# Performance work log

Measured on AMD Instinct MI355X. Metric: run time of the kernel, lower is better.

The kernel has to match this reference:

```python
import jax, jax.numpy as jnp
import numpy as np

N, E, G = 50000, 1600000, 512
IN_DIM, HEADS, C1, C2, HIDDEN = 128, 3, 32, 32, 512
NEG_SLOPE = 0.2
EPS = 1e-16


def _glorot(key, shape):
    fan_in = shape[0]
    return jax.random.normal(key, shape, dtype=jnp.float32) / np.sqrt(fan_in)


def setup_inputs() -> dict:
    key = jax.random.key(0)
    ks = jax.random.split(key, 16)
    x = jax.random.normal(ks[0], (N, IN_DIM), dtype=jnp.float32)
    edge_index = jax.random.randint(ks[1], (2, E), 0, N, dtype=jnp.int64)
    batch = (jnp.arange(N, dtype=jnp.int64) * G) // N  # sorted, all graphs non-empty
    d1, d2 = HEADS * C1, HEADS * C2
    return {
        "x": x,
        "W_l1": _glorot(ks[2], (IN_DIM, d1)), "b_l1": jnp.zeros((d1,), jnp.float32),
        "W_r1": _glorot(ks[3], (IN_DIM, d1)), "b_r1": jnp.zeros((d1,), jnp.float32),
        "att1": _glorot(ks[4], (HEADS, C1)), "bias1": jnp.zeros((d1,), jnp.float32),
        "W_l2": _glorot(ks[5], (d1, d2)), "b_l2": jnp.zeros((d2,), jnp.float32),
        "W_r2": _glorot(ks[6], (d1, d2)), "b_r2": jnp.zeros((d2,), jnp.float32),
        "att2": _glorot(ks[7], (HEADS, C2)), "bias2": jnp.zeros((d2,), jnp.float32),
        "W_fc1": _glorot(ks[8], (d1 + d2, HIDDEN)), "b_fc1": jnp.zeros((HIDDEN,), jnp.float32),
        "W_fc2": _glorot(ks[9], (HIDDEN, 2)), "b_fc2": jnp.zeros((2,), jnp.float32),
        "edge_index": edge_index,
        "batch": batch,
    }


def gatv2_conv(xin, src, dst, W_l, b_l, W_r, b_r, att, bias, heads, out_c):
    n = xin.shape[0]
    x_l = (xin @ W_l + b_l).reshape(n, heads, out_c)  # source-side projection
    x_r = (xin @ W_r + b_r).reshape(n, heads, out_c)  # target-side projection
    e = jax.nn.leaky_relu(x_l[src] + x_r[dst], NEG_SLOPE)  # [E', H, C]
    logits = jnp.einsum("ehc,hc->eh", e, att)  # [E', H]
    m = jax.ops.segment_max(logits, dst, num_segments=n)
    a = jnp.exp(logits - m[dst])
    denom = jax.ops.segment_sum(a, dst, num_segments=n)
    alpha = a / (denom[dst] + EPS)  # per-destination edge softmax (PyG semantics)
    out = jax.ops.segment_sum(x_l[src] * alpha[:, :, None], dst, num_segments=n)
    return out.reshape(n, heads * out_c) + bias


def reference(x, W_l1, b_l1, W_r1, b_r1, att1, bias1,
              W_l2, b_l2, W_r2, b_r2, att2, bias2,
              W_fc1, b_fc1, W_fc2, b_fc2, edge_index, batch):
    n = x.shape[0]
    loop = jnp.arange(n, dtype=edge_index.dtype)
    src = jnp.concatenate([edge_index[0], loop])  # PyG GATv2Conv adds self-loops
    dst = jnp.concatenate([edge_index[1], loop])
    h1 = jnp.tanh(gatv2_conv(x, src, dst, W_l1, b_l1, W_r1, b_r1, att1, bias1, HEADS, C1))
    h2 = jnp.tanh(gatv2_conv(h1, src, dst, W_l2, b_l2, W_r2, b_r2, att2, bias2, HEADS, C2))
    h = jnp.concatenate([h1, h2], axis=1)  # [N, (C1+C2)*H]
    first_idx = jnp.searchsorted(batch, jnp.arange(G, dtype=batch.dtype))  # first node of each graph
    pooled = h[first_idx]  # [G, (C1+C2)*H]
    hidden = jax.nn.relu(pooled @ W_fc1 + b_fc1)
    logits = hidden @ W_fc2 + b_fc2
    return jax.nn.log_softmax(logits, axis=1)
```

## Files before the change

kernel.cpp:

```cpp
#include <hip/hip_runtime.h>
#include <hip/hip_bf16.h>
#include <hip/hip_fp16.h>
#include <math.h>

#define NN 50000
#define EE 1600000
#define GG 512
#define INDIM 128
#define HEADS 3
#define CC 32
#define DD 96
#define HID 512
#define NEG 0.2f
#define NEGM1 (NEG - 1.0f)
#define EPS_DEN 1e-16f
#define CAP 128
#define NBW 1568
#define LOG2E 1.44269504f
#define PCLAMP2 86.5617f

#define PS_BL1   0
#define PS_BR1   96
#define PS_ATT1  192
#define PS_BIAS1 288
#define PS_BL2   384
#define PS_BR2   480
#define PS_ATT2  576
#define PS_BIAS2 672
#define PS_BFC1  768
#define PS_WFC2  1280
#define PS_BFC2  2304
#define PS_TOTAL 2308

typedef _Float16 h8 __attribute__((ext_vector_type(8)));
typedef float f4 __attribute__((ext_vector_type(4)));

static __device__ __forceinline__ float bf2f(__hip_bfloat16 v) { return __bfloat162float(v); }

static __device__ __forceinline__ int getI(const void* p, long long i, bool w64) {
    return w64 ? ((const int*)p)[2 * i] : ((const int*)p)[i];
}

static __device__ __forceinline__ float rawf(const void* p, int i, bool isbf) {
    return isbf ? bf2f(((const __hip_bfloat16*)p)[i]) : ((const float*)p)[i];
}

static __device__ __forceinline__ void load4(const void* p, int base, int e0, bool w64, int* v) {
    const int4* q = (const int4*)p;
    if (w64) {
        int4 a = q[(base + e0) >> 1];
        int4 b = q[((base + e0) >> 1) + 1];
        v[0] = a.x; v[1] = a.z; v[2] = b.x; v[3] = b.z;
    } else {
        int4 a = q[(base + e0) >> 2];
        v[0] = a.x; v[1] = a.y; v[2] = a.z; v[3] = a.w;
    }
}

static __device__ __forceinline__ bool testbit(const unsigned* b, int i) {
    return (b[i >> 5] >> (i & 31)) & 1u;
}

template <int CTRL>
static __device__ __forceinline__ float dpp_add(float v) {
    int t = __builtin_amdgcn_update_dpp(0, __float_as_int(v), CTRL, 0xF, 0xF, true);
    return v + __int_as_float(t);
}
static __device__ __forceinline__ float red16(float p) {
    p = dpp_add<0x121>(p);
    p = dpp_add<0x122>(p);
    p = dpp_add<0x124>(p);
    p = dpp_add<0x128>(p);
    return p;
}

static __device__ __forceinline__ float edge_e(float2 x, float2 xr2, float2 aa) {
    float t0 = x.x + xr2.x; t0 = fmaf(fminf(t0, 0.0f), NEGM1, t0);
    float t1 = x.y + xr2.y; t1 = fmaf(fminf(t1, 0.0f), NEGM1, t1);
    return exp2f(fminf(red16(fmaf(t1, aa.y, t0 * aa.x)), PCLAMP2));
}

__global__ void detect_kernel(const void* __restrict__ x, const void* __restrict__ ei,
                              int* __restrict__ flags)
{
    __shared__ int wild, zcnt;
    if (threadIdx.x == 0) { wild = 0; zcnt = 0; }
    __syncthreads();
    int w = 0, z = 0;
    const __hip_bfloat16* xb = (const __hip_bfloat16*)x;
    for (int i = threadIdx.x; i < 4096; i += 256) {
        float v = bf2f(xb[i]);
        if (!(fabsf(v) <= 1e6f)) w++;
    }
    const int* e32 = (const int*)ei;
    for (int i = threadIdx.x; i < 4096; i += 256) {
        if (e32[2 * i + 1] == 0) z++;
    }
    atomicAdd(&wild, w);
    atomicAdd(&zcnt, z);
    __syncthreads();
    if (threadIdx.x == 0) {
        flags[0] = (wild < 64) ? 1 : 0;
        flags[1] = (zcnt > 4000) ? 1 : 0;
    }
}

struct SetupArgs {
    const void *wl1, *wr1, *wl2, *wr2, *wfc1;
    const void *bl1, *br1, *att1, *bias1, *bl2, *br2, *att2, *bias2, *bfc1, *wfc2, *bfc2;
    const void *batch;
};

__global__ void setup_kernel(SetupArgs a, const int* __restrict__ flags,
                             float* __restrict__ P, __half* __restrict__ B1,
                             __half* __restrict__ B2, __half* __restrict__ Bfc,
                             int* __restrict__ deg, int* __restrict__ needed,
                             int* __restrict__ first, unsigned* __restrict__ pb,
                             int* __restrict__ cnt)
{
    const int task = blockIdx.y;
    const int idx = blockIdx.x * 256 + threadIdx.x;
    const bool isbf = flags[0] != 0;

    if (task == 0) {
        if (idx == 0) *cnt = 0;
        if (idx >= PS_TOTAL) return;
        const void* src; int rel;
        if (idx < 768) {
            int k = idx / 96; rel = idx - k * 96;
            const void* s8[8] = {a.bl1, a.br1, a.att1, a.bias1, a.bl2, a.br2, a.att2, a.bias2};
            src = s8[k];
        } else if (idx < 1280) { src = a.bfc1; rel = idx - 768; }
        else if (idx < 2304)   { src = a.wfc2; rel = idx - 1280; }
        else if (idx < 2306)   { src = a.bfc2; rel = idx - 2304; }
        else return;
        P[idx] = rawf(src, rel, isbf);
    } else if (task == 1 || task == 2) {
        const int KC = (task == 1) ? 4 : 3;
        const int total = 12 * KC * 64;
        if (idx >= total) return;
        int lane = idx & 63, t = idx >> 6;
        int kc = t % KC, ntile = t / KC;
        int n = ntile * 16 + (lane & 15);
        int kbase = kc * 32 + (lane >> 4) * 8;
        const void* W = (task == 1) ? (n < 96 ? a.wl1 : a.wr1) : (n < 96 ? a.wl2 : a.wr2);
        int n2 = (n < 96) ? n : n - 96;
        __half* dst = ((task == 1) ? B1 : B2) + (size_t)idx * 8;
#pragma unroll
        for (int j = 0; j < 8; j++) dst[j] = __float2half(rawf(W, (kbase + j) * 96 + n2, isbf));
    } else if (task == 3) {
        const int total = 32 * 6 * 64;
        if (idx >= total) return;
        int lane = idx & 63, t = idx >> 6;
        int kc = t % 6, ntile = t / 6;
        int n = ntile * 16 + (lane & 15);
        int kbase = kc * 32 + (lane >> 4) * 8;
        __half* dst = Bfc + (size_t)idx * 8;
#pragma unroll
        for (int j = 0; j < 8; j++) dst[j] = __float2half(rawf(a.wfc1, (kbase + j) * HID + n, isbf));
    } else if (task == 4) {
        int i0 = idx * 4;
#pragma unroll
        for (int j = 0; j < 4; j++) if (i0 + j < NN) deg[i0 + j] = 0;
    } else if (task == 5) {
        if (idx >= NN) return;
        const bool w64 = flags[1] != 0;
        int b = getI(a.batch, idx, w64);
        bool isf = (idx == 0) || (getI(a.batch, idx - 1, w64) != b);
        needed[idx] = isf ? 1 : 0;
        if (isf) first[b] = idx;
    } else {
        if (idx >= NBW) return;
        const bool w64 = flags[1] != 0;
        unsigned word = 0;
        int prev = (idx == 0) ? -1 : getI(a.batch, idx * 32 - 1, w64);
        for (int bit = 0; bit < 32; bit++) {
            int i = idx * 32 + bit;
            if (i >= NN) break;
            int b = getI(a.batch, i, w64);
            if (i == 0 || b != prev) word |= (1u << bit);
            prev = b;
        }
        pb[idx] = word;
    }
}

__global__ void mark_needed_kernel(const void* __restrict__ ei, const int* __restrict__ flags,
                                   const unsigned* __restrict__ pb, int* __restrict__ needed)
{
    int e0 = (blockIdx.x * 256 + threadIdx.x) * 4;
    if (e0 >= EE) return;
    const bool w64 = flags[1] != 0;
    int d4[4];
    load4(ei, EE, e0, w64, d4);
#pragma unroll
    for (int j = 0; j < 4; j++)
        if (testbit(pb, d4[j])) needed[getI(ei, e0 + j, w64)] = 1;
}

__global__ void scatter_compact_kernel(const void* __restrict__ ei, const int* __restrict__ flags,
                                       const int* __restrict__ needed,
                                       int* __restrict__ deg, int* __restrict__ csr,
                                       int* __restrict__ list, int* __restrict__ cnt)
{
    if (blockIdx.y == 1) {
        int i = blockIdx.x * 256 + threadIdx.x;
        if (i >= NN) return;
        if (needed[i]) list[atomicAdd(cnt, 1)] = i;
        return;
    }
    int e0 = (blockIdx.x * 256 + threadIdx.x) * 4;
    if (e0 >= EE) return;
    const bool w64 = flags[1] != 0;
    int s4[4], d4[4];
    load4(ei, EE, e0, w64, d4);
    load4(ei, 0, e0, w64, s4);
#pragma unroll
    for (int j = 0; j < 4; j++) {
        int dst = d4[j];
        if (!needed[dst]) continue;
        int pos = atomicAdd(&deg[dst], 1);
        if (pos < CAP) csr[(size_t)dst * CAP + pos] = s4[j];
    }
}

template <int KDIM, int MODE>
__global__ __launch_bounds__(256) void proj_mfma_kernel(
    const void* __restrict__ Ain, const __half* __restrict__ Bswz,
    const int* __restrict__ list, const int* __restrict__ cnt,
    const float* __restrict__ P, const int* __restrict__ flags, int offBl, int offBr,
    __half* __restrict__ xl, float* __restrict__ xr)
{
    constexpr int KC = KDIM / 32;
    __shared__ __half Bs[12 * KC * 64 * 8];
    const int tid = threadIdx.x;
    const int limit = MODE ? *cnt : NN;
    const int blockBase = blockIdx.x * 64;
    if (blockBase >= limit) return;

    {
        const int chunks = 12 * KC * 64;
        for (int i = tid; i < chunks; i += 256)
            reinterpret_cast<f4*>(Bs)[i] = reinterpret_cast<const f4*>(Bswz)[i];
    }
    __syncthreads();

    const int wave = tid >> 6;
    const int lane = tid & 63;
    const int base = blockBase + wave * 16;
    if (base >= limit) return;

    const int q = lane >> 4;
    const int mlane = lane & 15;

    int aIdx = base + mlane;
    int aRow;
    if (MODE) aRow = (aIdx < limit) ? list[aIdx] : list[limit - 1];
    else      aRow = (aIdx < limit) ? aIdx : 0;

    h8 a[KC];
    if (MODE == 1) {
        const h8* arow = reinterpret_cast<const h8*>((const __half*)Ain + (size_t)aRow * KDIM);
#pragma unroll
        for (int kc = 0; kc < KC; kc++) a[kc] = arow[kc * 4 + q];
    } else if (flags[0]) {
        const int4* arow = reinterpret_cast<const int4*>((const ushort*)Ain + (size_t)aRow * KDIM);
#pragma unroll
        for (int kc = 0; kc < KC; kc++) {
            int4 r = arow[kc * 4 + q];
            int ws[4] = {r.x, r.y, r.z, r.w};
#pragma unroll
            for (int i = 0; i < 4; i++) {
                a[kc][2 * i]     = (_Float16)__int_as_float(ws[i] << 16);
                a[kc][2 * i + 1] = (_Float16)__int_as_float(ws[i] & 0xffff0000);
            }
        }
    } else {
        const f4* arow = reinterpret_cast<const f4*>((const float*)Ain + (size_t)aRow * KDIM);
#pragma unroll
        for (int kc = 0; kc < KC; kc++) {
            f4 r0 = arow[kc * 8 + q * 2];
            f4 r1 = arow[kc * 8 + q * 2 + 1];
#pragma unroll
            for (int i = 0; i < 4; i++) {
                a[kc][i]     = (_Float16)r0[i];
                a[kc][4 + i] = (_Float16)r1[i];
            }
        }
    }

    int sRow[4];
#pragma unroll
    for (int r = 0; r < 4; r++) {
        int si = base + q * 4 + r;
        sRow[r] = (si < limit) ? (MODE ? list[si] : si) : -1;
    }

    const h8* Bf = reinterpret_cast<const h8*>(Bs);
#pragma unroll
    for (int ntile = 0; ntile < 12; ntile++) {
        int n = ntile * 16 + mlane;
        float bv = (n < 96) ? P[offBl + n] : P[offBr + n - 96];
        f4 acc = {bv, bv, bv, bv};
#pragma unroll
        for (int kc = 0; kc < KC; kc++) {
            h8 b = Bf[(ntile * KC + kc) * 64 + lane];
            acc = __builtin_amdgcn_mfma_f32_16x16x32_f16(a[kc], b, acc, 0, 0, 0);
        }
#pragma unroll
        for (int r = 0; r < 4; r++) {
            if (sRow[r] < 0) continue;
            if (n < 96) xl[(size_t)sRow[r] * DD + n] = __float2half(acc[r]);
            else        xr[(size_t)sRow[r] * DD + (n - 96)] = acc[r];
        }
    }
}

template <int OUTMODE>
__global__ __launch_bounds__(256) void fused_edge_kernel(
    const int* __restrict__ csr, const int* __restrict__ deg,
    const int* __restrict__ list, const int* __restrict__ cnt,
    const __half* __restrict__ xl, const float* __restrict__ xr,
    const float* __restrict__ P, int offAtt, int offBias,
    __half* __restrict__ out)
{
    const int lane = threadIdx.x & 63;
    const int g = lane >> 4;
    const int t = lane & 15;
    const int w0 = (blockIdx.x * 256 + threadIdx.x) >> 6;
    const int nw = (gridDim.x * 256) >> 6;
    const int limit = (OUTMODE == 0) ? *cnt : GG;

    float2 a_[3];
#pragma unroll
    for (int h = 0; h < 3; h++) {
        float2 av = *reinterpret_cast<const float2*>(P + offAtt + h * CC + 2 * t);
        a_[h].x = av.x * LOG2E; a_[h].y = av.y * LOG2E;
    }

    for (int li = w0; li < limit; li += nw) {
        const int n = list[li];
        const int* row = csr + (size_t)n * CAP;
        const int end = min(deg[n], CAP);
        const float* xrn = xr + (size_t)n * DD;
        float2 xr_[3];
#pragma unroll
        for (int h = 0; h < 3; h++) xr_[h] = *reinterpret_cast<const float2*>(xrn + h * CC + 2 * t);

        float d0, d1, d2, o00, o01, o10, o11, o20, o21;
        {
            const __half2* sp = reinterpret_cast<const __half2*>(xl + (size_t)n * DD) + t;
            float2 x0 = __half22float2(sp[0]);
            float2 x1 = __half22float2(sp[16]);
            float2 x2 = __half22float2(sp[32]);
            float e0 = edge_e(x0, xr_[0], a_[0]);
            float e1 = edge_e(x1, xr_[1], a_[1]);
            float e2 = edge_e(x2, xr_[2], a_[2]);
            if (g == 0) {
                d0 = e0; o00 = e0 * x0.x; o01 = e0 * x0.y;
                d1 = e1; o10 = e1 * x1.x; o11 = e1 * x1.y;
                d2 = e2; o20 = e2 * x2.x; o21 = e2 * x2.y;
            } else {
                d0 = d1 = d2 = 0.0f;
                o00 = o01 = o10 = o11 = o20 = o21 = 0.0f;
            }
        }

        int k = g;
        for (; k + 4 < end; k += 8) {
            int s0 = row[k], s1 = row[k + 4];
            const __half2* p0 = reinterpret_cast<const __half2*>(xl + (size_t)s0 * DD) + t;
            const __half2* p1 = reinterpret_cast<const __half2*>(xl + (size_t)s1 * DD) + t;
            __half2 ra0 = p0[0], ra1 = p0[16], ra2 = p0[32];
            __half2 rb0 = p1[0], rb1 = p1[16], rb2 = p1[32];
            float2 xa0 = __half22float2(ra0), xa1 = __half22float2(ra1), xa2 = __half22float2(ra2);
            float2 xb0 = __half22float2(rb0), xb1 = __half22float2(rb1), xb2 = __half22float2(rb2);
            float ea0 = edge_e(xa0, xr_[0], a_[0]);
            float ea1 = edge_e(xa1, xr_[1], a_[1]);
            float ea2 = edge_e(xa2, xr_[2], a_[2]);
            float eb0 = edge_e(xb0, xr_[0], a_[0]);
            float eb1 = edge_e(xb1, xr_[1], a_[1]);
            float eb2 = edge_e(xb2, xr_[2], a_[2]);
            d0 += ea0 + eb0; d1 += ea1 + eb1; d2 += ea2 + eb2;
            o00 = fmaf(ea0, xa0.x, o00); o00 = fmaf(eb0, xb0.x, o00);
            o01 = fmaf(ea0, xa0.y, o01); o01 = fmaf(eb0, xb0.y, o01);
            o10 = fmaf(ea1, xa1.x, o10); o10 = fmaf(eb1, xb1.x, o10);
            o11 = fmaf(ea1, xa1.y, o11); o11 = fmaf(eb1, xb1.y, o11);
            o20 = fmaf(ea2, xa2.x, o20); o20 = fmaf(eb2, xb2.x, o20);
            o21 = fmaf(ea2, xa2.y, o21); o21 = fmaf(eb2, xb2.y, o21);
        }
        for (; k < end; k += 4) {
            int s0 = row[k];
            const __half2* p0 = reinterpret_cast<const __half2*>(xl + (size_t)s0 * DD) + t;
            float2 xa0 = __half22float2(p0[0]);
            float2 xa1 = __half22float2(p0[16]);
            float2 xa2 = __half22float2(p0[32]);
            float ea0 = edge_e(xa0, xr_[0], a_[0]);
            float ea1 = edge_e(xa1, xr_[1], a_[1]);
            float ea2 = edge_e(xa2, xr_[2], a_[2]);
            d0 += ea0; d1 += ea1; d2 += ea2;
            o00 = fmaf(ea0, xa0.x, o00); o01 = fmaf(ea0, xa0.y, o01);
            o10 = fmaf(ea1, xa1.x, o10); o11 = fmaf(ea1, xa1.y, o11);
            o20 = fmaf(ea2, xa2.x, o20); o21 = fmaf(ea2, xa2.y, o21);
        }

        d0 += __shfl_xor(d0, 16); d0 += __shfl_xor(d0, 32);
        d1 += __shfl_xor(d1, 16); d1 += __shfl_xor(d1, 32);
        d2 += __shfl_xor(d2, 16); d2 += __shfl_xor(d2, 32);
        o00 += __shfl_xor(o00, 16); o00 += __shfl_xor(o00, 32);
        o01 += __shfl_xor(o01, 16); o01 += __shfl_xor(o01, 32);
        o10 += __shfl_xor(o10, 16); o10 += __shfl_xor(o10, 32);
        o11 += __shfl_xor(o11, 16); o11 += __shfl_xor(o11, 32);
        o20 += __shfl_xor(o20, 16); o20 += __shfl_xor(o20, 32);
        o21 += __shfl_xor(o21, 16); o21 += __shfl_xor(o21, 32);

        if (g == 0) {
            float inv0 = 1.0f / (d0 + EPS_DEN);
            float inv1 = 1.0f / (d1 + EPS_DEN);
            float inv2 = 1.0f / (d2 + EPS_DEN);
            float2 bv0 = *reinterpret_cast<const float2*>(P + offBias + 0 * CC + 2 * t);
            float2 bv1 = *reinterpret_cast<const float2*>(P + offBias + 1 * CC + 2 * t);
            float2 bv2 = *reinterpret_cast<const float2*>(P + offBias + 2 * CC + 2 * t);
            __half2 h0 = __floats2half2_rn(tanhf(fmaf(o00, inv0, bv0.x)), tanhf(fmaf(o01, inv0, bv0.y)));
            __half2 h1 = __floats2half2_rn(tanhf(fmaf(o10, inv1, bv1.x)), tanhf(fmaf(o11, inv1, bv1.y)));
            __half2 h2 = __floats2half2_rn(tanhf(fmaf(o20, inv2, bv2.x)), tanhf(fmaf(o21, inv2, bv2.y)));
            __half* ob = (OUTMODE == 0) ? (out + (size_t)n * DD) : (out + (size_t)li * DD);
            *reinterpret_cast<__half2*>(ob + 0 * CC + 2 * t) = h0;
            *reinterpret_cast<__half2*>(ob + 1 * CC + 2 * t) = h1;
            *reinterpret_cast<__half2*>(ob + 2 * CC + 2 * t) = h2;
        }
    }
}

__global__ __launch_bounds__(256) void mlp_mfma_kernel(
    const __half* __restrict__ h1h, const __half* __restrict__ A2,
    const int* __restrict__ first, const __half* __restrict__ Bfc,
    const float* __restrict__ P, const int* __restrict__ flags, void* __restrict__ outv)
{
    const int tid = threadIdx.x;
    const int wave = tid >> 6, lane = tid & 63;
    const int q = lane >> 4, ml = lane & 15;
    const int rowbase = blockIdx.x * 64 + wave * 16;
    const int g16 = rowbase + ml;

    h8 a[6];
    {
        const h8* l = reinterpret_cast<const h8*>(h1h + (size_t)first[g16] * DD);
#pragma unroll
        for (int kc = 0; kc < 3; kc++) a[kc] = l[kc * 4 + q];
        const h8* r = reinterpret_cast<const h8*>(A2 + (size_t)g16 * DD);
#pragma unroll
        for (int kc = 3; kc < 6; kc++) a[kc] = r[(kc - 3) * 4 + q];
    }

    const h8* Bf = reinterpret_cast<const h8*>(Bfc);
    const float* w2 = P + PS_WFC2;
    float p0[4] = {0, 0, 0, 0}, p1[4] = {0, 0, 0, 0};
    for (int nt = 0; nt < 32; nt++) {
        int n = nt * 16 + ml;
        float bv = P[PS_BFC1 + n];
        f4 acc = {bv, bv, bv, bv};
#pragma unroll
        for (int kc = 0; kc < 6; kc++)
            acc = __builtin_amdgcn_mfma_f32_16x16x32_f16(a[kc], Bf[(nt * 6 + kc) * 64 + lane], acc, 0, 0, 0);
        float w20 = w2[2 * n], w21 = w2[2 * n + 1];
#pragma unroll
        for (int r = 0; r < 4; r++) {
            float hdn = fmaxf(acc[r], 0.0f);
            p0[r] = fmaf(hdn, w20, p0[r]);
            p1[r] = fmaf(hdn, w21, p1[r]);
        }
    }
#pragma unroll
    for (int off = 1; off <= 8; off <<= 1) {
#pragma unroll
        for (int r = 0; r < 4; r++) {
            p0[r] += __shfl_xor(p0[r], off);
            p1[r] += __shfl_xor(p1[r], off);
        }
    }
    if (ml == 0) {
        float b0 = P[PS_BFC2], b1 = P[PS_BFC2 + 1];
#pragma unroll
        for (int r = 0; r < 4; r++) {
            int g = rowbase + q * 4 + r;
            float l0 = p0[r] + b0, l1 = p1[r] + b1;
            float mx = fmaxf(l0, l1);
            float lse = mx + logf(__expf(l0 - mx) + __expf(l1 - mx));
            if (flags[0]) {
                ((__hip_bfloat16*)outv)[g * 2 + 0] = __float2bfloat16(l0 - lse);
                ((__hip_bfloat16*)outv)[g * 2 + 1] = __float2bfloat16(l1 - lse);
            } else {
                ((float*)outv)[g * 2 + 0] = l0 - lse;
                ((float*)outv)[g * 2 + 1] = l1 - lse;
            }
        }
    }
}

extern "C" void kernel_launch(void* const* d_in, const int* in_sizes, int n_in,
                              void* d_out, int out_size, void* d_ws, size_t ws_size,
                              hipStream_t stream)
{
    const void* x     = d_in[0];
    const void* ei    = d_in[17];
    const void* batch = d_in[18];

    float* ws   = (float*)d_ws;
    float* P    = ws;
    float* xr   = P + PS_TOTAL;

    __half* hp   = (__half*)(xr + (size_t)NN * DD);
    __half* xlh  = hp;
    __half* xl2h = xlh + (size_t)NN * DD;
    __half* h1h  = xl2h + (size_t)NN * DD;
    __half* A2   = h1h + (size_t)NN * DD;
    __half* B1   = A2 + (size_t)GG * DD;
    __half* B2   = B1 + 24576;
    __half* Bfc  = B2 + 18432;

    int* ip       = (int*)(Bfc + 98304);
    int* deg      = ip;
    int* needed   = deg + NN;
    int* cnt      = needed + NN;
    int* csr      = cnt + 4;
    int* list     = csr + (size_t)NN * CAP;
    int* first    = list + NN;
    int* flags    = first + GG;
    unsigned* pb  = (unsigned*)(flags + 4);

    SetupArgs sa;
    sa.wl1 = d_in[1];  sa.bl1 = d_in[2];  sa.wr1 = d_in[3];  sa.br1 = d_in[4];
    sa.att1 = d_in[5]; sa.bias1 = d_in[6];
    sa.wl2 = d_in[7];  sa.bl2 = d_in[8];  sa.wr2 = d_in[9];  sa.br2 = d_in[10];
    sa.att2 = d_in[11]; sa.bias2 = d_in[12];
    sa.wfc1 = d_in[13]; sa.bfc1 = d_in[14]; sa.wfc2 = d_in[15]; sa.bfc2 = d_in[16];
    sa.batch = batch;

    const int edge4B = (EE / 4 + 255) / 256;
    const int mprojB = (NN + 63) / 64;
    const int fuse1B = 2048;
    const int fuse2B = GG / 4;

    detect_kernel<<<1, 256, 0, stream>>>(x, ei, flags);
    setup_kernel<<<dim3(196, 7), 256, 0, stream>>>(sa, flags, P, B1, B2, Bfc,
                                                   deg, needed, first, pb, cnt);
    mark_needed_kernel<<<edge4B, 256, 0, stream>>>(ei, flags, pb, needed);
    scatter_compact_kernel<<<dim3(edge4B, 2), 256, 0, stream>>>(ei, flags, needed,
                                                                deg, csr, list, cnt);

    proj_mfma_kernel<INDIM, 0><<<mprojB, 256, 0, stream>>>(x, B1, nullptr, nullptr,
                                                           P, flags, PS_BL1, PS_BR1, xlh, xr);
    fused_edge_kernel<0><<<fuse1B, 256, 0, stream>>>(csr, deg, list, cnt, xlh, xr,
                                                     P, PS_ATT1, PS_BIAS1, h1h);

    proj_mfma_kernel<DD, 1><<<mprojB, 256, 0, stream>>>(h1h, B2, list, cnt,
                                                        P, flags, PS_BL2, PS_BR2, xl2h, xr);
    fused_edge_kernel<1><<<fuse2B, 256, 0, stream>>>(csr, deg, first, nullptr, xl2h, xr,
                                                     P, PS_ATT2, PS_BIAS2, A2);

    mlp_mfma_kernel<<<GG / 64, 256, 0, stream>>>(h1h, A2, first, Bfc, P, flags, d_out);
}
```

Measured before the change: 259.8 us.

## Unroll edge gather to four neighbors, pre-scale CSR indices, early-exit scatter

The edge-aggregation loop now gathers four neighbor rows per iteration instead of two, which raises memory-level parallelism for the random xl gathers. CSR entries are stored pre-multiplied by the half2 row stride, so the inner loop avoids 64-bit index multiplies. The scatter kernel now checks whether any of the four destinations is needed before loading the source indices, so it can return early. The wider unroll uses more registers and may lower occupancy, and the pre-scaled index only fits in 32 bits for the current sizes.

```diff
diff --git a/kernel.cpp b/kernel.cpp
--- a/kernel.cpp
+++ b/kernel.cpp
@@ -214,13 +214,16 @@
     const bool w64 = flags[1] != 0;
     int s4[4], d4[4];
     load4(ei, EE, e0, w64, d4);
+    int nd0 = needed[d4[0]], nd1 = needed[d4[1]], nd2 = needed[d4[2]], nd3 = needed[d4[3]];
+    if (!(nd0 | nd1 | nd2 | nd3)) return;
     load4(ei, 0, e0, w64, s4);
+    int nd[4] = {nd0, nd1, nd2, nd3};
 #pragma unroll
     for (int j = 0; j < 4; j++) {
         int dst = d4[j];
-        if (!needed[dst]) continue;
+        if (!nd[j]) continue;
         int pos = atomicAdd(&deg[dst], 1);
-        if (pos < CAP) csr[(size_t)dst * CAP + pos] = s4[j];
+        if (pos < CAP) csr[(size_t)dst * CAP + pos] = s4[j] * (DD / 2);
     }
 }
 
@@ -330,6 +333,7 @@
     const int w0 = (blockIdx.x * 256 + threadIdx.x) >> 6;
     const int nw = (gridDim.x * 256) >> 6;
     const int limit = (OUTMODE == 0) ? *cnt : GG;
+    const __half2* xl2p = reinterpret_cast<const __half2*>(xl);
 
     float2 a_[3];
 #pragma unroll
@@ -349,7 +353,7 @@
 
         float d0, d1, d2, o00, o01, o10, o11, o20, o21;
         {
-            const __half2* sp = reinterpret_cast<const __half2*>(xl + (size_t)n * DD) + t;
+            const __half2* sp = xl2p + n * (DD / 2) + t;
             float2 x0 = __half22float2(sp[0]);
             float2 x1 = __half22float2(sp[16]);
             float2 x2 = __half22float2(sp[32]);
@@ -367,20 +371,44 @@
         }
 
         int k = g;
+        for (; k + 12 < end; k += 16) {
+            int s0 = row[k], s1 = row[k + 4], s2 = row[k + 8], s3 = row[k + 12];
+            const __half2* p0 = xl2p + s0 + t;
+            const __half2* p1 = xl2p + s1 + t;
+            const __half2* p2 = xl2p + s2 + t;
+            const __half2* p3 = xl2p + s3 + t;
+            __half2 r00 = p0[0], r01 = p0[16], r02 = p0[32];
+            __half2 r10 = p1[0], r11 = p1[16], r12 = p1[32];
+            __half2 r20 = p2[0], r21 = p2[16], r22 = p2[32];
+            __half2 r30 = p3[0], r31 = p3[16], r32 = p3[32];
+            float2 xa0 = __half22float2(r00), xa1 = __half22float2(r01), xa2 = __half22float2(r02);
+            float2 xb0 = __half22float2(r10), xb1 = __half22float2(r11), xb2 = __half22float2(r12);
+            float2 xc0 = __half22float2(r20), xc1 = __half22float2(r21), xc2 = __half22float2(r22);
+            float2 xd0 = __half22float2(r30), xd1 = __half22float2(r31), xd2 = __half22float2(r32);
+            float ea0 = edge_e(xa0, xr_[0], a_[0]), ea1 = edge_e(xa1, xr_[1], a_[1]), ea2 = edge_e(xa2, xr_[2], a_[2]);
+            float eb0 = edge_e(xb0, xr_[0], a_[0]), eb1 = edge_e(xb1, xr_[1], a_[1]), eb2 = edge_e(xb2, xr_[2], a_[2]);
+            float ec0 = edge_e(xc0, xr_[0], a_[0]), ec1 = edge_e(xc1, xr_[1], a_[1]), ec2 = edge_e(xc2, xr_[2], a_[2]);
+            float ed0 = edge_e(xd0, xr_[0], a_[0]), ed1 = edge_e(xd1, xr_[1], a_[1]), ed2 = edge_e(xd2, xr_[2], a_[2]);
+            d0 += (ea0 + eb0) + (ec0 + ed0);
+            d1 += (ea1 + eb1) + (ec1 + ed1);
+            d2 += (ea2 + eb2) + (ec2 + ed2);
+            o00 = fmaf(ea0, xa0.x, o00); o00 = fmaf(eb0, xb0.x, o00); o00 = fmaf(ec0, xc0.x, o00); o00 = fmaf(ed0, xd0.x, o00);
+            o01 = fmaf(ea0, xa0.y, o01); o01 = fmaf(eb0, xb0.y, o01); o01 = fmaf(ec0, xc0.y, o01); o01 = fmaf(ed0, xd0.y, o01);
+            o10 = fmaf(ea1, xa1.x, o10); o10 = fmaf(eb1, xb1.x, o10); o10 = fmaf(ec1, xc1.x, o10); o10 = fmaf(ed1, xd1.x, o10);
+            o11 = fmaf(ea1, xa1.y, o11); o11 = fmaf(eb1, xb1.y, o11); o11 = fmaf(ec1, xc1.y, o11); o11 = fmaf(ed1, xd1.y, o11);
+            o20 = fmaf(ea2, xa2.x, o20); o20 = fmaf(eb2, xb2.x, o20); o20 = fmaf(ec2, xc2.x, o20); o20 = fmaf(ed2, xd2.x, o20);
+            o21 = fmaf(ea2, xa2.y, o21); o21 = fmaf(eb2, xb2.y, o21); o21 = fmaf(ec2, xc2.y, o21); o21 = fmaf(ed2, xd2.y, o21);
+        }
         for (; k + 4 < end; k += 8) {
             int s0 = row[k], s1 = row[k + 4];
-            const __half2* p0 = reinterpret_cast<const __half2*>(xl + (size_t)s0 * DD) + t;
-            const __half2* p1 = reinterpret_cast<const __half2*>(xl + (size_t)s1 * DD) + t;
+            const __half2* p0 = xl2p + s0 + t;
+            const __half2* p1 = xl2p + s1 + t;
             __half2 ra0 = p0[0], ra1 = p0[16], ra2 = p0[32];
             __half2 rb0 = p1[0], rb1 = p1[16], rb2 = p1[32];
             float2 xa0 = __half22float2(ra0), xa1 = __half22float2(ra1), xa2 = __half22float2(ra2);
             float2 xb0 = __half22float2(rb0), xb1 = __half22float2(rb1), xb2 = __half22float2(rb2);
-            float ea0 = edge_e(xa0, xr_[0], a_[0]);
-            float ea1 = edge_e(xa1, xr_[1], a_[1]);
-            float ea2 = edge_e(xa2, xr_[2], a_[2]);
-            float eb0 = edge_e(xb0, xr_[0], a_[0]);
-            float eb1 = edge_e(xb1, xr_[1], a_[1]);
-            float eb2 = edge_e(xb2, xr_[2], a_[2]);
+            float ea0 = edge_e(xa0, xr_[0], a_[0]), ea1 = edge_e(xa1, xr_[1], a_[1]), ea2 = edge_e(xa2, xr_[2], a_[2]);
+            float eb0 = edge_e(xb0, xr_[0], a_[0]), eb1 = edge_e(xb1, xr_[1], a_[1]), eb2 = edge_e(xb2, xr_[2], a_[2]);
             d0 += ea0 + eb0; d1 += ea1 + eb1; d2 += ea2 + eb2;
             o00 = fmaf(ea0, xa0.x, o00); o00 = fmaf(eb0, xb0.x, o00);
             o01 = fmaf(ea0, xa0.y, o01); o01 = fmaf(eb0, xb0.y, o01);
@@ -391,7 +419,7 @@
         }
         for (; k < end; k += 4) {
             int s0 = row[k];
-            const __half2* p0 = reinterpret_cast<const __half2*>(xl + (size_t)s0 * DD) + t;
+            const __half2* p0 = xl2p + s0 + t;
             float2 xa0 = __half22float2(p0[0]);
             float2 xa1 = __half22float2(p0[16]);
             float2 xa2 = __half22float2(p0[32]);
```

Measured after the change: 259.8 us. No clear change (+0.0%).
